# Optimization experiments

Measured on AMD Instinct MI355X. Metric: run time of the kernel, lower is better.

## Reference

```python
import jax, jax.numpy as jnp
import numpy as np

NUM_NODES = 100_000
NUM_EDGES = 20_000
NNZ = 1_000_000


def setup_inputs() -> dict:
    key = jax.random.key(0)
    ks = jax.random.split(key, 8)
    d_in, d_hid, d_out = 128, 256, 40
    return {
        "x": jax.random.normal(ks[0], (NUM_NODES, d_in), dtype=jnp.float32),
        "node_idx": jax.random.randint(ks[1], (NNZ,), 0, NUM_NODES, dtype=jnp.int32),
        "edge_idx": jax.random.randint(ks[2], (NNZ,), 0, NUM_EDGES, dtype=jnp.int32),
        "W1": jax.random.normal(ks[3], (d_in, d_hid), dtype=jnp.float32) * (1.0 / np.sqrt(d_in)),
        "b1": jnp.zeros((d_hid,), dtype=jnp.float32),
        "W2": jax.random.normal(ks[4], (d_hid, d_hid), dtype=jnp.float32) * (1.0 / np.sqrt(d_hid)),
        "b2": jnp.zeros((d_hid,), dtype=jnp.float32),
        "W3": jax.random.normal(ks[5], (d_hid, d_out), dtype=jnp.float32) * (1.0 / np.sqrt(d_hid)),
        "b3": jnp.zeros((d_out,), dtype=jnp.float32),
    }


def _degree_norms(node_idx, edge_idx):
    # D = per-node incidence count (hyperedge_weight = ones); B = per-hyperedge node count
    ones = jnp.ones((node_idx.shape[0],), dtype=jnp.float32)
    D = jax.ops.segment_sum(ones, node_idx, num_segments=NUM_NODES)
    B = jax.ops.segment_sum(ones, edge_idx, num_segments=NUM_EDGES)
    Dinv = jnp.where(D > 0, 1.0 / D, 0.0)  # 1/D with inf -> 0, per PyG
    Binv = jnp.where(B > 0, 1.0 / B, 0.0)
    return Dinv, Binv


def _hconv(x, W, b, node_idx, edge_idx, Dinv, Binv):
    # PyG HypergraphConv (use_attention=False): X' = D^{-1} H B^{-1} H^T X W + b
    x = x @ W                                                            # [N, F]
    m = jax.ops.segment_sum(x[node_idx], edge_idx, num_segments=NUM_EDGES)  # H^T X W -> [E, F]
    m = Binv[:, None] * m
    out = jax.ops.segment_sum(m[edge_idx], node_idx, num_segments=NUM_NODES)  # [N, F]
    return Dinv[:, None] * out + b


def reference(x, node_idx, edge_idx, W1, b1, W2, b2, W3, b3):
    Dinv, Binv = _degree_norms(node_idx, edge_idx)
    # conv layers 0..L-2: conv -> ELU -> dropout (eval mode: identity)
    h = jax.nn.elu(_hconv(x, W1, b1, node_idx, edge_idx, Dinv, Binv))
    h = jax.nn.elu(_hconv(h, W2, b2, node_idx, edge_idx, Dinv, Binv))
    # final conv, no activation
    return _hconv(h, W3, b3, node_idx, edge_idx, Dinv, Binv)
```

## Files before the change

### kernel.cpp

```cpp
#include <hip/hip_runtime.h>
#include <cstdint>
#include <cstddef>

constexpr int N_NODES = 100000;
constexpr int N_EDGES = 20000;
constexpr int NNZ     = 1000000;
constexpr int NPAD    = 100096;
constexpr int EPAD    = 20096;

typedef __attribute__((ext_vector_type(8))) __bf16 bf16x8;
typedef __attribute__((ext_vector_type(4))) float f32x4;

__device__ __forceinline__ unsigned short bf16_rne(float v) {
  unsigned u = __builtin_bit_cast(unsigned, v);
  return (unsigned short)((u + 0x7FFFu + ((u >> 16) & 1u)) >> 16);
}
__device__ __forceinline__ void split2(float v, unsigned short& h, unsigned short& l) {
  unsigned u = __builtin_bit_cast(unsigned, v);
  unsigned hb = (u + 0x7FFFu + ((u >> 16) & 1u)) & 0xFFFF0000u;
  h = (unsigned short)(hb >> 16);
  float lo = v - __builtin_bit_cast(float, hb);
  l = bf16_rne(lo);
}
__device__ __forceinline__ float elu_f(float x) { return x > 0.f ? x : expm1f(x); }

__device__ __forceinline__ void gload_lds16(const void* g, void* l) {
  __builtin_amdgcn_global_load_lds(
      (const __attribute__((address_space(1))) unsigned int*)(uintptr_t)g,
      (__attribute__((address_space(3))) unsigned int*)(uintptr_t)l, 16, 0, 0);
}

__global__ void count_kernel(const int* __restrict__ ni, const int* __restrict__ ei,
                             int* __restrict__ dcnt, int* __restrict__ bcnt) {
  int i = blockIdx.x * blockDim.x + threadIdx.x;
  if (i < NNZ) {
    atomicAdd(&dcnt[ni[i]], 1);
    atomicAdd(&bcnt[ei[i]], 1);
  }
}

__global__ void invert2_kernel(const int* __restrict__ dcnt, const int* __restrict__ bcnt,
                               float* __restrict__ dinv, float* __restrict__ binv) {
  int i = blockIdx.x * blockDim.x + threadIdx.x;
  if (i < N_NODES) {
    int c = dcnt[i];
    dinv[i] = c > 0 ? 1.0f / (float)c : 0.0f;
  }
  if (i < N_EDGES) {
    int c = bcnt[i];
    binv[i] = c > 0 ? 1.0f / (float)c : 0.0f;
  }
}

__device__ __forceinline__ void scan_block_body(const int* __restrict__ cnt, int n,
                                                int* __restrict__ out,
                                                int* __restrict__ partials, int bid) {
  __shared__ int buf[256];
  int tid = threadIdx.x;
  int i = bid * 256 + tid;
  int v = (i < n) ? cnt[i] : 0;
  buf[tid] = v;
  __syncthreads();
  for (int o = 1; o < 256; o <<= 1) {
    int t = (tid >= o) ? buf[tid - o] : 0;
    __syncthreads();
    buf[tid] += t;
    __syncthreads();
  }
  if (i < n) out[i] = buf[tid] - v;
  if (tid == 255) partials[bid] = buf[tid];
}

__global__ void scan_block2(const int* __restrict__ c1, int n1, int* __restrict__ o1,
                            int* __restrict__ p1, int nb1,
                            const int* __restrict__ c2, int n2, int* __restrict__ o2,
                            int* __restrict__ p2) {
  if ((int)blockIdx.x < nb1) scan_block_body(c1, n1, o1, p1, blockIdx.x);
  else scan_block_body(c2, n2, o2, p2, blockIdx.x - nb1);
}

__device__ __forceinline__ void scan_partials_body(int* __restrict__ partials, int nb,
                                                   int* __restrict__ total_out) {
  __shared__ int buf[1024];
  int tid = threadIdx.x;
  int v = (tid < nb) ? partials[tid] : 0;
  buf[tid] = v;
  __syncthreads();
  for (int o = 1; o < 1024; o <<= 1) {
    int t = (tid >= o) ? buf[tid - o] : 0;
    __syncthreads();
    buf[tid] += t;
    __syncthreads();
  }
  if (tid < nb) partials[tid] = buf[tid] - v;
  if (tid == 1023) *total_out = buf[1023];
}

__global__ void scan_partials2(int* __restrict__ p1, int nb1, int* __restrict__ t1,
                               int* __restrict__ p2, int nb2, int* __restrict__ t2) {
  if (blockIdx.x == 0) scan_partials_body(p1, nb1, t1);
  else scan_partials_body(p2, nb2, t2);
}

__global__ void scan_add2(int* __restrict__ o1, int n1, const int* __restrict__ p1, int nb1,
                          int* __restrict__ o2, int n2, const int* __restrict__ p2) {
  if ((int)blockIdx.x < nb1) {
    int i = blockIdx.x * 256 + threadIdx.x;
    if (i < n1) o1[i] += p1[blockIdx.x];
  } else {
    int b = blockIdx.x - nb1;
    int i = b * 256 + threadIdx.x;
    if (i < n2) o2[i] += p2[b];
  }
}

__global__ void fill_kernel(const int* __restrict__ ni, const int* __restrict__ ei,
                            const int* __restrict__ noff, const int* __restrict__ eoff,
                            int* __restrict__ ncur, int* __restrict__ ecur,
                            int* __restrict__ nedges, int* __restrict__ enodes) {
  int i = blockIdx.x * blockDim.x + threadIdx.x;
  if (i < NNZ) {
    int n = ni[i], e = ei[i];
    int p = atomicAdd(&ecur[e], 1);
    enodes[eoff[e] + p] = n;
    int q = atomicAdd(&ncur[n], 1);
    nedges[noff[n] + q] = e;
  }
}

__global__ void wsplit_all(const float* __restrict__ W1, const float* __restrict__ W2,
                           const float* __restrict__ W3,
                           unsigned short* __restrict__ W1th, unsigned short* __restrict__ W1tl,
                           unsigned short* __restrict__ W2th, unsigned short* __restrict__ W2tl,
                           unsigned short* __restrict__ W3th, unsigned short* __restrict__ W3tl) {
  int i = blockIdx.x * 256 + threadIdx.x;
  float v;
  unsigned short h, l;
  if (i < 32768) {
    int n = i >> 7, k = i & 127;
    v = W1[(size_t)k * 256 + n];
    split2(v, h, l);
    W1th[i] = h; W1tl[i] = l;
  } else if (i < 98304) {
    int j = i - 32768;
    int n = j >> 8, k = j & 255;
    v = W2[(size_t)k * 256 + n];
    split2(v, h, l);
    W2th[j] = h; W2tl[j] = l;
  } else if (i < 110592) {
    int j = i - 98304;
    int n = j >> 8, k = j & 255;
    v = (n < 40) ? W3[(size_t)k * 40 + n] : 0.0f;
    split2(v, h, l);
    W3th[j] = h; W3tl[j] = l;
  }
}

template <int MFR, int NFR, int WAVES_M, int WAVES_N, int EPI>
__global__ __launch_bounds__(256) void gemm_tile(
    const unsigned short* __restrict__ Ah, const unsigned short* __restrict__ Al,
    const unsigned short* __restrict__ Bh, const unsigned short* __restrict__ Bl,
    int K, const float* __restrict__ bias, float* __restrict__ outF, int ncols,
    int Mrows) {
  constexpr int BM = WAVES_M * MFR * 16;
  constexpr int BN = WAVES_N * NFR * 16;
  __shared__ char lds[(BM + BN) * 128];
  char* Ash = lds;
  char* Asl = lds + BM * 64;
  char* Bsh = lds + BM * 128;
  char* Bsl = lds + BM * 128 + BN * 64;

  const int wave = threadIdx.x >> 6;
  const int lane = threadIdx.x & 63;
  const int rl = lane & 15;
  const int g = lane >> 4;
  const int wr = wave / WAVES_N;
  const int wc = wave % WAVES_N;
  const int rowbase = blockIdx.x * BM;
  const int colbase = blockIdx.y * BN;

  f32x4 acc[MFR][NFR] = {};

  auto stage = [&](const unsigned short* G, char* S, int R, int rbase, int k0) {
    for (int wi = wave; wi < (R >> 4); wi += 4) {
      int c = wi * 64 + lane;
      int row = c >> 2;
      int colbyte = ((lane & 3) * 16) ^ ((row & 3) << 4);
      const char* src = (const char*)G + ((size_t)(rbase + row) * K + k0) * 2 + colbyte;
      gload_lds16(src, S + wi * 1024);
    }
  };

  for (int k0 = 0; k0 < K; k0 += 32) {
    stage(Ah, Ash, BM, rowbase, k0);
    stage(Al, Asl, BM, rowbase, k0);
    stage(Bh, Bsh, BN, colbase, k0);
    stage(Bl, Bsl, BN, colbase, k0);
    asm volatile("s_waitcnt vmcnt(0)" ::: "memory");
    __syncthreads();

    bf16x8 afh[MFR], afl[MFR], bfh[NFR], bfl[NFR];
#pragma unroll
    for (int mf = 0; mf < MFR; ++mf) {
      int r = wr * MFR * 16 + mf * 16 + rl;
      int addr = r * 64 + ((g * 16) ^ ((r & 3) << 4));
      afh[mf] = *(const bf16x8*)(Ash + addr);
      afl[mf] = *(const bf16x8*)(Asl + addr);
    }
#pragma unroll
    for (int nf = 0; nf < NFR; ++nf) {
      int r = wc * NFR * 16 + nf * 16 + rl;
      int addr = r * 64 + ((g * 16) ^ ((r & 3) << 4));
      bfh[nf] = *(const bf16x8*)(Bsh + addr);
      bfl[nf] = *(const bf16x8*)(Bsl + addr);
    }
#pragma unroll
    for (int mf = 0; mf < MFR; ++mf)
#pragma unroll
      for (int nf = 0; nf < NFR; ++nf) {
        acc[mf][nf] = __builtin_amdgcn_mfma_f32_16x16x32_bf16(afh[mf], bfh[nf], acc[mf][nf], 0, 0, 0);
        acc[mf][nf] = __builtin_amdgcn_mfma_f32_16x16x32_bf16(afh[mf], bfl[nf], acc[mf][nf], 0, 0, 0);
        acc[mf][nf] = __builtin_amdgcn_mfma_f32_16x16x32_bf16(afl[mf], bfh[nf], acc[mf][nf], 0, 0, 0);
      }
    __syncthreads();
  }

#pragma unroll
  for (int mf = 0; mf < MFR; ++mf)
#pragma unroll
    for (int nf = 0; nf < NFR; ++nf)
#pragma unroll
      for (int i = 0; i < 4; ++i) {
        int grow = rowbase + wr * MFR * 16 + mf * 16 + g * 4 + i;
        if (grow >= Mrows) continue;
        int gcol = colbase + wc * NFR * 16 + nf * 16 + rl;
        if (gcol >= ncols) continue;
        float v = acc[mf][nf][i];
        if (EPI == 2) {
          v += bias[gcol];
          v = elu_f(v);
        }
        outF[(size_t)grow * ncols + gcol] = v;
      }
}

#define ACC4(a, v) { a.x += v.x; a.y += v.y; a.z += v.z; a.w += v.w; }

__global__ __launch_bounds__(256) void edge_reduce256_split(
    const float* __restrict__ h1, const int* __restrict__ eoff,
    const int* __restrict__ enodes, const float* __restrict__ binv,
    unsigned short* __restrict__ mh, unsigned short* __restrict__ ml) {
  int w = (blockIdx.x * blockDim.x + threadIdx.x) >> 6;
  int lane = threadIdx.x & 63;
  if (w >= EPAD) return;
  if (w >= N_EDGES) {
    uint2 z = {0, 0};
    *reinterpret_cast<uint2*>(&mh[(size_t)w * 256 + lane * 4]) = z;
    *reinterpret_cast<uint2*>(&ml[(size_t)w * 256 + lane * 4]) = z;
    return;
  }
  int s = eoff[w], t = eoff[w + 1];
  float4 a0 = {0, 0, 0, 0}, a1 = {0, 0, 0, 0}, a2 = {0, 0, 0, 0}, a3 = {0, 0, 0, 0};
  int j = s;
  for (; j < t && (j & 3); ++j) {
    float4 v = *reinterpret_cast<const float4*>(&h1[(size_t)enodes[j] * 256 + lane * 4]);
    ACC4(a0, v);
  }
  for (; j + 4 <= t; j += 4) {
    int4 idx = *reinterpret_cast<const int4*>(enodes + j);
    float4 v0 = *reinterpret_cast<const float4*>(&h1[(size_t)idx.x * 256 + lane * 4]);
    float4 v1 = *reinterpret_cast<const float4*>(&h1[(size_t)idx.y * 256 + lane * 4]);
    float4 v2 = *reinterpret_cast<const float4*>(&h1[(size_t)idx.z * 256 + lane * 4]);
    float4 v3 = *reinterpret_cast<const float4*>(&h1[(size_t)idx.w * 256 + lane * 4]);
    ACC4(a0, v0); ACC4(a1, v1); ACC4(a2, v2); ACC4(a3, v3);
  }
  for (; j < t; ++j) {
    float4 v = *reinterpret_cast<const float4*>(&h1[(size_t)enodes[j] * 256 + lane * 4]);
    ACC4(a0, v);
  }
  float bv = binv[w];
  float v0 = (a0.x + a1.x + a2.x + a3.x) * bv;
  float v1 = (a0.y + a1.y + a2.y + a3.y) * bv;
  float v2 = (a0.z + a1.z + a2.z + a3.z) * bv;
  float v3 = (a0.w + a1.w + a2.w + a3.w) * bv;
  unsigned short h0, l0, h1s, l1, h2, l2, h3, l3;
  split2(v0, h0, l0);
  split2(v1, h1s, l1);
  split2(v2, h2, l2);
  split2(v3, h3, l3);
  uint2 ph, pl;
  ph.x = (unsigned)h0 | ((unsigned)h1s << 16);
  ph.y = (unsigned)h2 | ((unsigned)h3 << 16);
  pl.x = (unsigned)l0 | ((unsigned)l1 << 16);
  pl.y = (unsigned)l2 | ((unsigned)l3 << 16);
  *reinterpret_cast<uint2*>(&mh[(size_t)w * 256 + lane * 4]) = ph;
  *reinterpret_cast<uint2*>(&ml[(size_t)w * 256 + lane * 4]) = pl;
}

__global__ __launch_bounds__(256) void node_reduce256_split_elu(
    const float* __restrict__ m, const int* __restrict__ noff,
    const int* __restrict__ nedges, const float* __restrict__ dinv,
    const float* __restrict__ bias, unsigned short* __restrict__ Ah,
    unsigned short* __restrict__ Al) {
  int w = (blockIdx.x * blockDim.x + threadIdx.x) >> 6;
  int lane = threadIdx.x & 63;
  if (w >= N_NODES) return;
  int s = noff[w], t = noff[w + 1];
  float4 a0 = {0, 0, 0, 0}, a1 = {0, 0, 0, 0}, a2 = {0, 0, 0, 0}, a3 = {0, 0, 0, 0};
  int j = s;
  for (; j < t && (j & 3); ++j) {
    float4 v = *reinterpret_cast<const float4*>(&m[(size_t)nedges[j] * 256 + lane * 4]);
    ACC4(a0, v);
  }
  for (; j + 4 <= t; j += 4) {
    int4 idx = *reinterpret_cast<const int4*>(nedges + j);
    float4 v0 = *reinterpret_cast<const float4*>(&m[(size_t)idx.x * 256 + lane * 4]);
    float4 v1 = *reinterpret_cast<const float4*>(&m[(size_t)idx.y * 256 + lane * 4]);
    float4 v2 = *reinterpret_cast<const float4*>(&m[(size_t)idx.z * 256 + lane * 4]);
    float4 v3 = *reinterpret_cast<const float4*>(&m[(size_t)idx.w * 256 + lane * 4]);
    ACC4(a0, v0); ACC4(a1, v1); ACC4(a2, v2); ACC4(a3, v3);
  }
  for (; j < t; ++j) {
    float4 v = *reinterpret_cast<const float4*>(&m[(size_t)nedges[j] * 256 + lane * 4]);
    ACC4(a0, v);
  }
  float dv = dinv[w];
  float4 b4 = *reinterpret_cast<const float4*>(&bias[lane * 4]);
  float v0 = elu_f((a0.x + a1.x + a2.x + a3.x) * dv + b4.x);
  float v1 = elu_f((a0.y + a1.y + a2.y + a3.y) * dv + b4.y);
  float v2 = elu_f((a0.z + a1.z + a2.z + a3.z) * dv + b4.z);
  float v3 = elu_f((a0.w + a1.w + a2.w + a3.w) * dv + b4.w);
  unsigned short h0, l0, h1, l1, h2, l2, h3, l3;
  split2(v0, h0, l0);
  split2(v1, h1, l1);
  split2(v2, h2, l2);
  split2(v3, h3, l3);
  uint2 ph, pl;
  ph.x = (unsigned)h0 | ((unsigned)h1 << 16);
  ph.y = (unsigned)h2 | ((unsigned)h3 << 16);
  pl.x = (unsigned)l0 | ((unsigned)l1 << 16);
  pl.y = (unsigned)l2 | ((unsigned)l3 << 16);
  *reinterpret_cast<uint2*>(&Ah[(size_t)w * 256 + lane * 4]) = ph;
  *reinterpret_cast<uint2*>(&Al[(size_t)w * 256 + lane * 4]) = pl;
}

__global__ __launch_bounds__(256) void edge_reduce128(const float* __restrict__ x,
                                                      const int* __restrict__ eoff,
                                                      const int* __restrict__ enodes,
                                                      const float* __restrict__ binv,
                                                      float* __restrict__ m) {
  int w = (blockIdx.x * blockDim.x + threadIdx.x) >> 6;
  int lane = threadIdx.x & 63;
  if (w >= N_EDGES) return;
  int s = eoff[w], t = eoff[w + 1];
  float2 a0 = {0, 0}, a1 = {0, 0}, a2 = {0, 0}, a3 = {0, 0};
  int j = s;
  for (; j < t && (j & 3); ++j) {
    float2 v = *reinterpret_cast<const float2*>(&x[(size_t)enodes[j] * 128 + lane * 2]);
    a0.x += v.x; a0.y += v.y;
  }
  for (; j + 4 <= t; j += 4) {
    int4 idx = *reinterpret_cast<const int4*>(enodes + j);
    float2 v0 = *reinterpret_cast<const float2*>(&x[(size_t)idx.x * 128 + lane * 2]);
    float2 v1 = *reinterpret_cast<const float2*>(&x[(size_t)idx.y * 128 + lane * 2]);
    float2 v2 = *reinterpret_cast<const float2*>(&x[(size_t)idx.z * 128 + lane * 2]);
    float2 v3 = *reinterpret_cast<const float2*>(&x[(size_t)idx.w * 128 + lane * 2]);
    a0.x += v0.x; a0.y += v0.y;
    a1.x += v1.x; a1.y += v1.y;
    a2.x += v2.x; a2.y += v2.y;
    a3.x += v3.x; a3.y += v3.y;
  }
  for (; j < t; ++j) {
    float2 v = *reinterpret_cast<const float2*>(&x[(size_t)enodes[j] * 128 + lane * 2]);
    a0.x += v.x; a0.y += v.y;
  }
  float bv = binv[w];
  float2 r;
  r.x = (a0.x + a1.x + a2.x + a3.x) * bv;
  r.y = (a0.y + a1.y + a2.y + a3.y) * bv;
  *reinterpret_cast<float2*>(&m[(size_t)w * 128 + lane * 2]) = r;
}

__global__ __launch_bounds__(256) void node_reduce128_split(const float* __restrict__ m,
                                                            const int* __restrict__ noff,
                                                            const int* __restrict__ nedges,
                                                            const float* __restrict__ dinv,
                                                            unsigned short* __restrict__ Ah,
                                                            unsigned short* __restrict__ Al) {
  int w = (blockIdx.x * blockDim.x + threadIdx.x) >> 6;
  int lane = threadIdx.x & 63;
  if (w >= N_NODES) return;
  int s = noff[w], t = noff[w + 1];
  float2 a0 = {0, 0}, a1 = {0, 0}, a2 = {0, 0}, a3 = {0, 0};
  int j = s;
  for (; j < t && (j & 3); ++j) {
    float2 v = *reinterpret_cast<const float2*>(&m[(size_t)nedges[j] * 128 + lane * 2]);
    a0.x += v.x; a0.y += v.y;
  }
  for (; j + 4 <= t; j += 4) {
    int4 idx = *reinterpret_cast<const int4*>(nedges + j);
    float2 v0 = *reinterpret_cast<const float2*>(&m[(size_t)idx.x * 128 + lane * 2]);
    float2 v1 = *reinterpret_cast<const float2*>(&m[(size_t)idx.y * 128 + lane * 2]);
    float2 v2 = *reinterpret_cast<const float2*>(&m[(size_t)idx.z * 128 + lane * 2]);
    float2 v3 = *reinterpret_cast<const float2*>(&m[(size_t)idx.w * 128 + lane * 2]);
    a0.x += v0.x; a0.y += v0.y;
    a1.x += v1.x; a1.y += v1.y;
    a2.x += v2.x; a2.y += v2.y;
    a3.x += v3.x; a3.y += v3.y;
  }
  for (; j < t; ++j) {
    float2 v = *reinterpret_cast<const float2*>(&m[(size_t)nedges[j] * 128 + lane * 2]);
    a0.x += v.x; a0.y += v.y;
  }
  float dv = dinv[w];
  float ax = (a0.x + a1.x + a2.x + a3.x) * dv;
  float ay = (a0.y + a1.y + a2.y + a3.y) * dv;
  unsigned short h0, l0, h1, l1;
  split2(ax, h0, l0);
  split2(ay, h1, l1);
  unsigned ph = (unsigned)h0 | ((unsigned)h1 << 16);
  unsigned pl = (unsigned)l0 | ((unsigned)l1 << 16);
  *reinterpret_cast<unsigned*>(&Ah[(size_t)w * 128 + lane * 2]) = ph;
  *reinterpret_cast<unsigned*>(&Al[(size_t)w * 128 + lane * 2]) = pl;
}

__global__ __launch_bounds__(256) void edge_reduce40(const float* __restrict__ xw,
                                                     const int* __restrict__ eoff,
                                                     const int* __restrict__ enodes,
                                                     const float* __restrict__ binv,
                                                     float* __restrict__ m) {
  int w = (blockIdx.x * blockDim.x + threadIdx.x) >> 6;
  int lane = threadIdx.x & 63;
  if (w >= N_EDGES || lane >= 40) return;
  int s = eoff[w], t = eoff[w + 1];
  float a0 = 0.f, a1 = 0.f, a2 = 0.f, a3 = 0.f;
  int j = s;
  for (; j < t && (j & 3); ++j) a0 += xw[(size_t)enodes[j] * 40 + lane];
  for (; j + 4 <= t; j += 4) {
    int4 idx = *reinterpret_cast<const int4*>(enodes + j);
    a0 += xw[(size_t)idx.x * 40 + lane];
    a1 += xw[(size_t)idx.y * 40 + lane];
    a2 += xw[(size_t)idx.z * 40 + lane];
    a3 += xw[(size_t)idx.w * 40 + lane];
  }
  for (; j < t; ++j) a0 += xw[(size_t)enodes[j] * 40 + lane];
  m[(size_t)w * 40 + lane] = (a0 + a1 + a2 + a3) * binv[w];
}

__global__ __launch_bounds__(256) void node_reduce40(const float* __restrict__ m,
                                                     const int* __restrict__ noff,
                                                     const int* __restrict__ nedges,
                                                     const float* __restrict__ dinv,
                                                     const float* __restrict__ bias,
                                                     float* __restrict__ out) {
  int w = (blockIdx.x * blockDim.x + threadIdx.x) >> 6;
  int lane = threadIdx.x & 63;
  if (w >= N_NODES || lane >= 40) return;
  int s = noff[w], t = noff[w + 1];
  float a0 = 0.f, a1 = 0.f, a2 = 0.f, a3 = 0.f;
  int j = s;
  for (; j < t && (j & 3); ++j) a0 += m[(size_t)nedges[j] * 40 + lane];
  for (; j + 4 <= t; j += 4) {
    int4 idx = *reinterpret_cast<const int4*>(nedges + j);
    a0 += m[(size_t)idx.x * 40 + lane];
    a1 += m[(size_t)idx.y * 40 + lane];
    a2 += m[(size_t)idx.z * 40 + lane];
    a3 += m[(size_t)idx.w * 40 + lane];
  }
  for (; j < t; ++j) a0 += m[(size_t)nedges[j] * 40 + lane];
  out[(size_t)w * 40 + lane] = (a0 + a1 + a2 + a3) * dinv[w] + bias[lane];
}

extern "C" void kernel_launch(void* const* d_in, const int* in_sizes, int n_in,
                              void* d_out, int out_size, void* d_ws, size_t ws_size,
                              hipStream_t stream) {
  const float* x  = (const float*)d_in[0];
  const int*   ni = (const int*)d_in[1];
  const int*   ei = (const int*)d_in[2];
  const float* W1 = (const float*)d_in[3];
  const float* b1 = (const float*)d_in[4];
  const float* W2 = (const float*)d_in[5];
  const float* b2 = (const float*)d_in[6];
  const float* W3 = (const float*)d_in[7];
  const float* b3 = (const float*)d_in[8];
  float* out = (float*)d_out;

  char* base = (char*)d_ws;
  size_t off = 0;
  auto take = [&](size_t bytes) -> char* {
    char* p = base + off;
    off += (bytes + 255) & ~(size_t)255;
    return p;
  };

  int* dcnt   = (int*)take((size_t)N_NODES * 4);
  int* bcnt   = (int*)take((size_t)N_EDGES * 4);
  int* ncur   = (int*)take((size_t)N_NODES * 4);
  int* ecur   = (int*)take((size_t)N_EDGES * 4);
  const size_t memset_span = 400128 + 80128 + 400128 + 80128;
  int* noff   = (int*)take((size_t)(N_NODES + 1) * 4);
  int* eoff   = (int*)take((size_t)(N_EDGES + 1) * 4);
  int* npart  = (int*)take((size_t)((N_NODES + 255) / 256) * 4);
  int* epart  = (int*)take((size_t)((N_EDGES + 255) / 256) * 4);
  int* nedges = (int*)take((size_t)NNZ * 4);
  int* enodes = (int*)take((size_t)NNZ * 4);
  float* dinv = (float*)take((size_t)N_NODES * 4);
  float* binv = (float*)take((size_t)N_EDGES * 4);

  unsigned short* W1th = (unsigned short*)take((size_t)256 * 128 * 2);
  unsigned short* W1tl = (unsigned short*)take((size_t)256 * 128 * 2);
  unsigned short* W2th = (unsigned short*)take((size_t)256 * 256 * 2);
  unsigned short* W2tl = (unsigned short*)take((size_t)256 * 256 * 2);
  unsigned short* W3th = (unsigned short*)take((size_t)48 * 256 * 2);
  unsigned short* W3tl = (unsigned short*)take((size_t)48 * 256 * 2);

  const size_t A2B = (size_t)NPAD * 256 * 2;
  char* R2 = take(2 * A2B);
  char* R3 = take(2 * A2B);

  float* h1 = (float*)R2;
  unsigned short* A3h = (unsigned short*)R2;
  unsigned short* A3l = (unsigned short*)(R2 + A2B);

  float* m128 = (float*)R3;
  unsigned short* A1h = (unsigned short*)(R3 + 10240000);
  unsigned short* A1l = (unsigned short*)(R3 + 10240000 + (size_t)NPAD * 128 * 2);

  const size_t MEB = (size_t)EPAD * 256 * 2;
  unsigned short* m2eh = (unsigned short*)R3;
  unsigned short* m2el = (unsigned short*)(R3 + MEB);
  float* m256f = (float*)(R3 + 2 * MEB);

  float* t3  = (float*)R3;
  float* m40 = (float*)(R3 + 16015360);

  hipMemsetAsync(dcnt, 0, memset_span, stream);
  count_kernel<<<(NNZ + 255) / 256, 256, 0, stream>>>(ni, ei, dcnt, bcnt);
  invert2_kernel<<<(N_NODES + 255) / 256, 256, 0, stream>>>(dcnt, bcnt, dinv, binv);

  const int nb_n = (N_NODES + 255) / 256;
  const int nb_e = (N_EDGES + 255) / 256;
  scan_block2<<<nb_n + nb_e, 256, 0, stream>>>(dcnt, N_NODES, noff, npart, nb_n,
                                               bcnt, N_EDGES, eoff, epart);
  scan_partials2<<<2, 1024, 0, stream>>>(npart, nb_n, &noff[N_NODES],
                                         epart, nb_e, &eoff[N_EDGES]);
  scan_add2<<<nb_n + nb_e, 256, 0, stream>>>(noff, N_NODES, npart, nb_n,
                                             eoff, N_EDGES, epart);
  fill_kernel<<<(NNZ + 255) / 256, 256, 0, stream>>>(ni, ei, noff, eoff, ncur, ecur, nedges, enodes);

  wsplit_all<<<(110592 + 255) / 256, 256, 0, stream>>>(W1, W2, W3, W1th, W1tl,
                                                       W2th, W2tl, W3th, W3tl);

  const int eblocks  = (N_EDGES * 64 + 255) / 256;
  const int epblocks = (EPAD * 64 + 255) / 256;
  const int nblocks  = (N_NODES * 64 + 255) / 256;
  const int gm  = NPAD / 128;
  const int gme = EPAD / 128;

  edge_reduce128<<<eblocks, 256, 0, stream>>>(x, eoff, enodes, binv, m128);
  node_reduce128_split<<<nblocks, 256, 0, stream>>>(m128, noff, nedges, dinv, A1h, A1l);
  gemm_tile<4, 4, 2, 2, 2><<<dim3(gm, 2), 256, 0, stream>>>(
      A1h, A1l, W1th, W1tl, 128, b1, h1, 256, N_NODES);

  edge_reduce256_split<<<epblocks, 256, 0, stream>>>(h1, eoff, enodes, binv, m2eh, m2el);
  gemm_tile<4, 4, 2, 2, 0><<<dim3(gme, 2), 256, 0, stream>>>(
      m2eh, m2el, W2th, W2tl, 256, nullptr, m256f, 256, N_EDGES);
  node_reduce256_split_elu<<<nblocks, 256, 0, stream>>>(m256f, noff, nedges, dinv, b2, A3h, A3l);

  gemm_tile<2, 3, 4, 1, 0><<<dim3(gm, 1), 256, 0, stream>>>(
      A3h, A3l, W3th, W3tl, 256, nullptr, t3, 40, N_NODES);
  edge_reduce40<<<eblocks, 256, 0, stream>>>(t3, eoff, enodes, binv, m40);
  node_reduce40<<<nblocks, 256, 0, stream>>>(m40, noff, nedges, dinv, b3, out);
}
```

Measured before the change: 812.9 us.

## Fuse count with weight split, fold inversion into scan, pad final layer to 48

Merges the degree-counting kernel with the weight bf16-split kernel, and computes the inverse degrees inside the scan kernel, which removes two launches. The final-layer GEMM output and the edge messages now use a 48-float row stride instead of 40, so rows are better aligned for the gathers. The last two gather-reduce kernels unroll to eight accumulators for more memory-level parallelism. The padded stride adds some extra bytes per row and relies on the GEMM writing 48 columns correctly.

```diff
diff --git a/kernel.cpp b/kernel.cpp
--- a/kernel.cpp
+++ b/kernel.cpp
@@ -30,35 +30,56 @@
       (__attribute__((address_space(3))) unsigned int*)(uintptr_t)l, 16, 0, 0);
 }
 
-__global__ void count_kernel(const int* __restrict__ ni, const int* __restrict__ ei,
-                             int* __restrict__ dcnt, int* __restrict__ bcnt) {
-  int i = blockIdx.x * blockDim.x + threadIdx.x;
-  if (i < NNZ) {
-    atomicAdd(&dcnt[ni[i]], 1);
-    atomicAdd(&bcnt[ei[i]], 1);
-  }
-}
-
-__global__ void invert2_kernel(const int* __restrict__ dcnt, const int* __restrict__ bcnt,
-                               float* __restrict__ dinv, float* __restrict__ binv) {
-  int i = blockIdx.x * blockDim.x + threadIdx.x;
-  if (i < N_NODES) {
-    int c = dcnt[i];
-    dinv[i] = c > 0 ? 1.0f / (float)c : 0.0f;
-  }
-  if (i < N_EDGES) {
-    int c = bcnt[i];
-    binv[i] = c > 0 ? 1.0f / (float)c : 0.0f;
+constexpr int COUNT_BLOCKS = (NNZ + 255) / 256;
+
+__global__ void count_wsplit(const int* __restrict__ ni, const int* __restrict__ ei,
+                             int* __restrict__ dcnt, int* __restrict__ bcnt,
+                             const float* __restrict__ W1, const float* __restrict__ W2,
+                             const float* __restrict__ W3,
+                             unsigned short* __restrict__ W1th, unsigned short* __restrict__ W1tl,
+                             unsigned short* __restrict__ W2th, unsigned short* __restrict__ W2tl,
+                             unsigned short* __restrict__ W3th, unsigned short* __restrict__ W3tl) {
+  int b = blockIdx.x;
+  if (b < COUNT_BLOCKS) {
+    int i = b * 256 + threadIdx.x;
+    if (i < NNZ) {
+      atomicAdd(&dcnt[ni[i]], 1);
+      atomicAdd(&bcnt[ei[i]], 1);
+    }
+  } else {
+    int i = (b - COUNT_BLOCKS) * 256 + threadIdx.x;
+    float v;
+    unsigned short h, l;
+    if (i < 32768) {
+      int n = i >> 7, k = i & 127;
+      v = W1[(size_t)k * 256 + n];
+      split2(v, h, l);
+      W1th[i] = h; W1tl[i] = l;
+    } else if (i < 98304) {
+      int j = i - 32768;
+      int n = j >> 8, k = j & 255;
+      v = W2[(size_t)k * 256 + n];
+      split2(v, h, l);
+      W2th[j] = h; W2tl[j] = l;
+    } else if (i < 110592) {
+      int j = i - 98304;
+      int n = j >> 8, k = j & 255;
+      v = (n < 40) ? W3[(size_t)k * 40 + n] : 0.0f;
+      split2(v, h, l);
+      W3th[j] = h; W3tl[j] = l;
+    }
   }
 }
 
 __device__ __forceinline__ void scan_block_body(const int* __restrict__ cnt, int n,
                                                 int* __restrict__ out,
-                                                int* __restrict__ partials, int bid) {
+                                                int* __restrict__ partials, int bid,
+                                                float* __restrict__ inv) {
   __shared__ int buf[256];
   int tid = threadIdx.x;
   int i = bid * 256 + tid;
   int v = (i < n) ? cnt[i] : 0;
+  if (i < n) inv[i] = v > 0 ? 1.0f / (float)v : 0.0f;
   buf[tid] = v;
   __syncthreads();
   for (int o = 1; o < 256; o <<= 1) {
@@ -74,9 +95,10 @@
 __global__ void scan_block2(const int* __restrict__ c1, int n1, int* __restrict__ o1,
                             int* __restrict__ p1, int nb1,
                             const int* __restrict__ c2, int n2, int* __restrict__ o2,
-                            int* __restrict__ p2) {
-  if ((int)blockIdx.x < nb1) scan_block_body(c1, n1, o1, p1, blockIdx.x);
-  else scan_block_body(c2, n2, o2, p2, blockIdx.x - nb1);
+                            int* __restrict__ p2,
+                            float* __restrict__ dinv, float* __restrict__ binv) {
+  if ((int)blockIdx.x < nb1) scan_block_body(c1, n1, o1, p1, blockIdx.x, dinv);
+  else scan_block_body(c2, n2, o2, p2, blockIdx.x - nb1, binv);
 }
 
 __device__ __forceinline__ void scan_partials_body(int* __restrict__ partials, int nb,
@@ -125,34 +147,6 @@
     enodes[eoff[e] + p] = n;
     int q = atomicAdd(&ncur[n], 1);
     nedges[noff[n] + q] = e;
-  }
-}
-
-__global__ void wsplit_all(const float* __restrict__ W1, const float* __restrict__ W2,
-                           const float* __restrict__ W3,
-                           unsigned short* __restrict__ W1th, unsigned short* __restrict__ W1tl,
-                           unsigned short* __restrict__ W2th, unsigned short* __restrict__ W2tl,
-                           unsigned short* __restrict__ W3th, unsigned short* __restrict__ W3tl) {
-  int i = blockIdx.x * 256 + threadIdx.x;
-  float v;
-  unsigned short h, l;
-  if (i < 32768) {
-    int n = i >> 7, k = i & 127;
-    v = W1[(size_t)k * 256 + n];
-    split2(v, h, l);
-    W1th[i] = h; W1tl[i] = l;
-  } else if (i < 98304) {
-    int j = i - 32768;
-    int n = j >> 8, k = j & 255;
-    v = W2[(size_t)k * 256 + n];
-    split2(v, h, l);
-    W2th[j] = h; W2tl[j] = l;
-  } else if (i < 110592) {
-    int j = i - 98304;
-    int n = j >> 8, k = j & 255;
-    v = (n < 40) ? W3[(size_t)k * 40 + n] : 0.0f;
-    split2(v, h, l);
-    W3th[j] = h; W3tl[j] = l;
   }
 }
 
@@ -424,7 +418,7 @@
   *reinterpret_cast<unsigned*>(&Al[(size_t)w * 128 + lane * 2]) = pl;
 }
 
-__global__ __launch_bounds__(256) void edge_reduce40(const float* __restrict__ xw,
+__global__ __launch_bounds__(256) void edge_reduce48(const float* __restrict__ xw,
                                                      const int* __restrict__ eoff,
                                                      const int* __restrict__ enodes,
                                                      const float* __restrict__ binv,
@@ -433,21 +427,26 @@
   int lane = threadIdx.x & 63;
   if (w >= N_EDGES || lane >= 40) return;
   int s = eoff[w], t = eoff[w + 1];
-  float a0 = 0.f, a1 = 0.f, a2 = 0.f, a3 = 0.f;
+  float a0 = 0.f, a1 = 0.f, a2 = 0.f, a3 = 0.f, a4 = 0.f, a5 = 0.f, a6 = 0.f, a7 = 0.f;
   int j = s;
-  for (; j < t && (j & 3); ++j) a0 += xw[(size_t)enodes[j] * 40 + lane];
-  for (; j + 4 <= t; j += 4) {
-    int4 idx = *reinterpret_cast<const int4*>(enodes + j);
-    a0 += xw[(size_t)idx.x * 40 + lane];
-    a1 += xw[(size_t)idx.y * 40 + lane];
-    a2 += xw[(size_t)idx.z * 40 + lane];
-    a3 += xw[(size_t)idx.w * 40 + lane];
-  }
-  for (; j < t; ++j) a0 += xw[(size_t)enodes[j] * 40 + lane];
-  m[(size_t)w * 40 + lane] = (a0 + a1 + a2 + a3) * binv[w];
-}
-
-__global__ __launch_bounds__(256) void node_reduce40(const float* __restrict__ m,
+  for (; j < t && (j & 7); ++j) a0 += xw[(size_t)enodes[j] * 48 + lane];
+  for (; j + 8 <= t; j += 8) {
+    int4 i0 = *reinterpret_cast<const int4*>(enodes + j);
+    int4 i1 = *reinterpret_cast<const int4*>(enodes + j + 4);
+    a0 += xw[(size_t)i0.x * 48 + lane];
+    a1 += xw[(size_t)i0.y * 48 + lane];
+    a2 += xw[(size_t)i0.z * 48 + lane];
+    a3 += xw[(size_t)i0.w * 48 + lane];
+    a4 += xw[(size_t)i1.x * 48 + lane];
+    a5 += xw[(size_t)i1.y * 48 + lane];
+    a6 += xw[(size_t)i1.z * 48 + lane];
+    a7 += xw[(size_t)i1.w * 48 + lane];
+  }
+  for (; j < t; ++j) a0 += xw[(size_t)enodes[j] * 48 + lane];
+  m[(size_t)w * 48 + lane] = ((a0 + a1) + (a2 + a3) + ((a4 + a5) + (a6 + a7))) * binv[w];
+}
+
+__global__ __launch_bounds__(256) void node_reduce48(const float* __restrict__ m,
                                                      const int* __restrict__ noff,
                                                      const int* __restrict__ nedges,
                                                      const float* __restrict__ dinv,
@@ -457,18 +456,23 @@
   int lane = threadIdx.x & 63;
   if (w >= N_NODES || lane >= 40) return;
   int s = noff[w], t = noff[w + 1];
-  float a0 = 0.f, a1 = 0.f, a2 = 0.f, a3 = 0.f;
+  float a0 = 0.f, a1 = 0.f, a2 = 0.f, a3 = 0.f, a4 = 0.f, a5 = 0.f, a6 = 0.f, a7 = 0.f;
   int j = s;
-  for (; j < t && (j & 3); ++j) a0 += m[(size_t)nedges[j] * 40 + lane];
-  for (; j + 4 <= t; j += 4) {
-    int4 idx = *reinterpret_cast<const int4*>(nedges + j);
-    a0 += m[(size_t)idx.x * 40 + lane];
-    a1 += m[(size_t)idx.y * 40 + lane];
-    a2 += m[(size_t)idx.z * 40 + lane];
-    a3 += m[(size_t)idx.w * 40 + lane];
-  }
-  for (; j < t; ++j) a0 += m[(size_t)nedges[j] * 40 + lane];
-  out[(size_t)w * 40 + lane] = (a0 + a1 + a2 + a3) * dinv[w] + bias[lane];
+  for (; j < t && (j & 7); ++j) a0 += m[(size_t)nedges[j] * 48 + lane];
+  for (; j + 8 <= t; j += 8) {
+    int4 i0 = *reinterpret_cast<const int4*>(nedges + j);
+    int4 i1 = *reinterpret_cast<const int4*>(nedges + j + 4);
+    a0 += m[(size_t)i0.x * 48 + lane];
+    a1 += m[(size_t)i0.y * 48 + lane];
+    a2 += m[(size_t)i0.z * 48 + lane];
+    a3 += m[(size_t)i0.w * 48 + lane];
+    a4 += m[(size_t)i1.x * 48 + lane];
+    a5 += m[(size_t)i1.y * 48 + lane];
+    a6 += m[(size_t)i1.z * 48 + lane];
+    a7 += m[(size_t)i1.w * 48 + lane];
+  }
+  for (; j < t; ++j) a0 += m[(size_t)nedges[j] * 48 + lane];
+  out[(size_t)w * 40 + lane] = ((a0 + a1) + (a2 + a3) + ((a4 + a5) + (a6 + a7))) * dinv[w] + bias[lane];
 }
 
 extern "C" void kernel_launch(void* const* d_in, const int* in_sizes, int n_in,
@@ -532,25 +536,22 @@
   float* m256f = (float*)(R3 + 2 * MEB);
 
   float* t3  = (float*)R3;
-  float* m40 = (float*)(R3 + 16015360);
+  float* m48 = (float*)(R3 + 19200000);
 
   hipMemsetAsync(dcnt, 0, memset_span, stream);
-  count_kernel<<<(NNZ + 255) / 256, 256, 0, stream>>>(ni, ei, dcnt, bcnt);
-  invert2_kernel<<<(N_NODES + 255) / 256, 256, 0, stream>>>(dcnt, bcnt, dinv, binv);
+  count_wsplit<<<COUNT_BLOCKS + (110592 + 255) / 256, 256, 0, stream>>>(
+      ni, ei, dcnt, bcnt, W1, W2, W3, W1th, W1tl, W2th, W2tl, W3th, W3tl);
 
   const int nb_n = (N_NODES + 255) / 256;
   const int nb_e = (N_EDGES + 255) / 256;
   scan_block2<<<nb_n + nb_e, 256, 0, stream>>>(dcnt, N_NODES, noff, npart, nb_n,
-                                               bcnt, N_EDGES, eoff, epart);
+                                               bcnt, N_EDGES, eoff, epart, dinv, binv);
   scan_partials2<<<2, 1024, 0, stream>>>(npart, nb_n, &noff[N_NODES],
                                          epart, nb_e, &eoff[N_EDGES]);
   scan_add2<<<nb_n + nb_e, 256, 0, stream>>>(noff, N_NODES, npart, nb_n,
                                              eoff, N_EDGES, epart);
   fill_kernel<<<(NNZ + 255) / 256, 256, 0, stream>>>(ni, ei, noff, eoff, ncur, ecur, nedges, enodes);
 
-  wsplit_all<<<(110592 + 255) / 256, 256, 0, stream>>>(W1, W2, W3, W1th, W1tl,
-                                                       W2th, W2tl, W3th, W3tl);
-
   const int eblocks  = (N_EDGES * 64 + 255) / 256;
   const int epblocks = (EPAD * 64 + 255) / 256;
   const int nblocks  = (N_NODES * 64 + 255) / 256;
@@ -568,7 +569,7 @@
   node_reduce256_split_elu<<<nblocks, 256, 0, stream>>>(m256f, noff, nedges, dinv, b2, A3h, A3l);
 
   gemm_tile<2, 3, 4, 1, 0><<<dim3(gm, 1), 256, 0, stream>>>(
-      A3h, A3l, W3th, W3tl, 256, nullptr, t3, 40, N_NODES);
-  edge_reduce40<<<eblocks, 256, 0, stream>>>(t3, eoff, enodes, binv, m40);
-  node_reduce40<<<nblocks, 256, 0, stream>>>(m40, noff, nedges, dinv, b3, out);
-}
+      A3h, A3l, W3th, W3tl, 256, nullptr, t3, 48, N_NODES);
+  edge_reduce48<<<eblocks, 256, 0, stream>>>(t3, eoff, enodes, binv, m48);
+  node_reduce48<<<nblocks, 256, 0, stream>>>(m48, noff, nedges, dinv, b3, out);
+}
```

Measured after the change: 831.2 us. 2.3% more time.
